# Kernel tuning notes

Hardware: AMD Instinct MI355X
Metric: run time of the kernel (lower is better)

Reference implementation:

```python
import math
import jax, jax.numpy as jnp
import numpy as np

NUM_ANGLE = 8
NUM_RADIAL = 3
RADIAL_MIN = 0.08
RADIAL_MAX = 0.9
EPS = 1e-6


def _hann(n):
    # torch.hann_window(n, periodic=False)
    return 0.5 * (1.0 - jnp.cos(2.0 * jnp.pi * jnp.arange(n, dtype=jnp.float32) / (n - 1)))


def _to_luma(img):
    # img: [B, 3, H, W] -> [B, H, W]
    return 0.2989 * img[:, 0] + 0.587 * img[:, 1] + 0.114 * img[:, 2]


def _log_magnitude(img):
    x = _to_luma(img).astype(jnp.float32)  # [B, H, W]
    H, W = x.shape[-2], x.shape[-1]
    win = _hann(H)[:, None] * _hann(W)[None, :]  # [H, W]
    x = x * win
    spec = jnp.fft.fftshift(jnp.fft.fft2(x, axes=(-2, -1)), axes=(-2, -1))
    return jnp.log1p(jnp.abs(spec))  # [B, H, W]


def _polar_masks(H, W):
    y = jnp.linspace(-1.0, 1.0, H, dtype=jnp.float32)
    x = jnp.linspace(-1.0, 1.0, W, dtype=jnp.float32)
    yy, xx = jnp.meshgrid(y, x, indexing='ij')
    radius = jnp.sqrt(xx * xx + yy * yy)
    radius = radius / jnp.maximum(radius.max(), EPS)
    angle = jnp.remainder(jnp.arctan2(yy, xx), math.pi)

    r_edges = jnp.linspace(RADIAL_MIN, RADIAL_MAX, NUM_RADIAL + 1, dtype=jnp.float32)
    a_edges = jnp.linspace(0.0, math.pi, NUM_ANGLE + 1, dtype=jnp.float32)

    r0 = r_edges[:-1][:, None, None]
    r1 = r_edges[1:][:, None, None]
    rmask = (radius[None] >= r0) & (radius[None] < r1)           # [R, H, W]
    rmask = rmask.at[-1].set((radius >= r_edges[-2]) & (radius <= r_edges[-1]))

    t0 = a_edges[:-1][:, None, None]
    t1 = a_edges[1:][:, None, None]
    amask = (angle[None] >= t0) & (angle[None] < t1)             # [A, H, W]
    amask = amask.at[-1].set((angle >= a_edges[-2]) & (angle <= a_edges[-1]))

    return (rmask[:, None] & amask[None, :]).astype(jnp.float32)  # [R, A, H, W]


def _sector_energies(img):
    mag = _log_magnitude(img)                          # [B, H, W]
    masks = _polar_masks(mag.shape[-2], mag.shape[-1])  # [R, A, H, W]
    mask_sum = jnp.maximum(masks.sum(axis=(-2, -1)), EPS)        # [R, A]
    masked_sum = jnp.einsum('bhw,rahw->bra', mag, masks)         # [B, R, A]
    energies = masked_sum / mask_sum[None]
    energies = energies / jnp.maximum(energies.sum(axis=-1, keepdims=True), EPS)
    return energies


def setup_inputs() -> dict:
    key = jax.random.key(0)
    k1, k2 = jax.random.split(key)
    B, C, H, W = 16, 3, 512, 512
    prediction = jax.random.uniform(k1, (B, C, H, W), dtype=jnp.float32)
    target = jax.random.uniform(k2, (B, C, H, W), dtype=jnp.float32)
    radial_weights = jnp.array([0.5, 1.0, 1.2], dtype=jnp.float32).reshape(1, NUM_RADIAL, 1)
    return {"prediction": prediction, "target": target, "radial_weights": radial_weights}


def reference(prediction, target, radial_weights):
    pred_e = _sector_energies(prediction)   # [B, R, A]
    tgt_e = _sector_energies(target)
    diff = pred_e - tgt_e
    dist = jnp.sqrt(diff * diff + EPS)      # charbonnier
    return (dist * radial_weights).mean()
```

## Files before the change

### kernel.cpp

```cpp
#include <hip/hip_runtime.h>
#include <math.h>

#define PI_F 3.14159265358979323846f
#define TWO_PI_F 6.28318530717958647692f
#define RSQ2 0.70710678118654752440f

#define LGKM(n) __asm__ volatile("s_waitcnt lgkmcnt(" #n ")" ::: "memory")
#define LADDR(a) ((a) + ((a) >> 3))

__device__ __forceinline__ float2 cadd(float2 a, float2 b){ return make_float2(a.x+b.x, a.y+b.y); }
__device__ __forceinline__ float2 csub(float2 a, float2 b){ return make_float2(a.x-b.x, a.y-b.y); }
__device__ __forceinline__ float2 cmul(float2 a, float2 b){ return make_float2(a.x*b.x - a.y*b.y, a.x*b.y + a.y*b.x); }
__device__ __forceinline__ float2 cw1(float2 a){ return make_float2(RSQ2*(a.x+a.y), RSQ2*(a.y-a.x)); }
__device__ __forceinline__ float2 cw2(float2 a){ return make_float2(a.y, -a.x); }
__device__ __forceinline__ float2 cw3(float2 a){ return make_float2(RSQ2*(a.y-a.x), -RSQ2*(a.x+a.y)); }

__device__ __forceinline__ void dft8(float2* v){
    float2 a0=cadd(v[0],v[4]), a1=cadd(v[1],v[5]), a2=cadd(v[2],v[6]), a3=cadd(v[3],v[7]);
    float2 b0=csub(v[0],v[4]);
    float2 b1=cw1(csub(v[1],v[5]));
    float2 b2=cw2(csub(v[2],v[6]));
    float2 b3=cw3(csub(v[3],v[7]));
    float2 c0=cadd(a0,a2), c2=csub(a0,a2), c1=cadd(a1,a3), c3=cw2(csub(a1,a3));
    float2 d0=cadd(b0,b2), d2=csub(b0,b2), d1=cadd(b1,b3), d3=cw2(csub(b1,b3));
    v[0]=cadd(c0,c1); v[1]=csub(c0,c1);
    v[2]=cadd(c2,c3); v[3]=csub(c2,c3);
    v[4]=cadd(d0,d1); v[5]=csub(d0,d1);
    v[6]=cadd(d2,d3); v[7]=csub(d2,d3);
}

__device__ __forceinline__ void calc_pows(float2 w, float2* p){
    p[0] = w;
    p[1] = cmul(w, w);
    p[2] = cmul(p[1], w);
    p[3] = cmul(p[1], p[1]);
    p[4] = cmul(p[2], p[1]);
    p[5] = cmul(p[2], p[2]);
    p[6] = cmul(p[3], p[2]);
}

__device__ __forceinline__ void stage_store(float2* wl, const float2* v, const float2* p,
                                            int base, int step){
    constexpr int br[8] = {0,4,2,6,1,5,3,7};
    wl[LADDR(base)] = v[0];
    #pragma unroll
    for (int c = 1; c < 8; ++c) wl[LADDR(base + step*c)] = cmul(v[br[c]], p[c-1]);
}

__device__ __forceinline__ void stage_load(const float2* wl, float2* v, int j){
    #pragma unroll
    for (int i = 0; i < 8; ++i) v[i] = wl[LADDR(j + 64*i)];
}

__device__ __forceinline__ void fft512_pair(float2* va, float2* vb,
                                            float2* wlA, float2* wlB,
                                            float2 tw0, float2 tw1, int j){
    float2 pw[7];
    calc_pows(tw0, pw);
    dft8(va);
    dft8(vb);
    stage_store(wlA, va, pw, 8 * j, 1);
    stage_store(wlB, vb, pw, 8 * j, 1);
    LGKM(8);
    stage_load(wlA, va, j);
    LGKM(8);
    stage_load(wlB, vb, j);
    LGKM(8);
    calc_pows(tw1, pw);
    dft8(va);
    stage_store(wlA, va, pw, (j & 7) + 64 * (j >> 3), 8);
    LGKM(8);
    dft8(vb);
    stage_store(wlB, vb, pw, (j & 7) + 64 * (j >> 3), 8);
    LGKM(8);
    stage_load(wlA, va, j);
    LGKM(8);
    stage_load(wlB, vb, j);
    LGKM(8);
    dft8(va);
    LGKM(0);
    dft8(vb);
}

__device__ __forceinline__ int sector_id(int hm, int wm) {
    const float step = 2.0f / 511.0f;
    float y = -1.0f + step * (float)hm;
    float x = -1.0f + step * (float)wm;
    float radius = sqrtf(x * x + y * y);
    float r = radius / sqrtf(2.0f);
    float a = atan2f(y, x);
    a = fmodf(a, PI_F);
    if (a < 0.0f) a += PI_F;

    const float rstep = (0.9f - 0.08f) / 3.0f;
    const float re0 = 0.08f;
    const float re1 = 0.08f + rstep;
    const float re2 = 0.08f + 2.0f * rstep;
    const float re3 = 0.9f;
    int rb;
    if      (r >= re0 && r < re1)  rb = 0;
    else if (r >= re1 && r < re2)  rb = 1;
    else if (r >= re2 && r <= re3) rb = 2;
    else return -1;

    const float astep = PI_F / 8.0f;
    int ab = 7;
    #pragma unroll
    for (int i = 0; i < 7; ++i) {
        float t0 = astep * (float)i;
        float t1 = astep * (float)(i + 1);
        if (a >= t0 && a < t1) { ab = i; break; }
    }
    return rb * 8 + ab;
}

__device__ __forceinline__ float hannf(int i) {
    return 0.5f * (1.0f - __cosf(TWO_PI_F * (float)i / 511.0f));
}

__device__ __forceinline__ float lumaf(const float* b, size_t off){
    return 0.2989f*b[off] + 0.587f*b[off+262144] + 0.114f*b[off+524288];
}

__device__ __forceinline__ void write_row_T(float4* __restrict__ out4, size_t ibase, int hp,
                                            const float2* v, int partner, int j){
    constexpr int br[8] = {0,4,2,6,1,5,3,7};
    float4* row = out4 + (ibase + (size_t)hp) * 256;
    #pragma unroll
    for (int c = 0; c < 4; ++c) {
        int k = j + 64 * c;
        float2 zk = v[br[c]];
        float mx = __shfl(v[br[7 - c]].x, partner, 64);
        float my = __shfl(v[br[7 - c]].y, partner, 64);
        float2 zs = v[br[(8 - c) & 7]];
        float2 zm = make_float2(j == 0 ? zs.x : mx, j == 0 ? zs.y : my);
        float4 o = make_float4(0.5f*(zk.x+zm.x), 0.5f*(zk.y-zm.y),
                               0.5f*(zk.y+zm.y), 0.5f*(zm.x-zk.x));
        if (k != 0) row[k] = o;
    }
    if (j == 0) {
        float2 z0 = v[br[0]], z4 = v[br[4]];
        row[0] = make_float4(z0.x, z4.x, z0.y, z4.y);
    }
}

__device__ __forceinline__ void bin_col(const float2* v,
                                        const unsigned char* __restrict__ mw1,
                                        const unsigned char* __restrict__ mw2,
                                        float* wb, int rep, int j){
    constexpr int br[8] = {0,4,2,6,1,5,3,7};
    #pragma unroll
    for (int c = 0; c < 8; ++c) {
        float2 z = v[br[c]];
        float mag = __logf(1.0f + sqrtf(z.x * z.x + z.y * z.y));
        int hm = j + 64 * ((c + 4) & 7);
        int s1 = mw1[hm]; if (s1 < 24) atomicAdd(&wb[rep + s1], mag);
        int hm2 = (256 - (j + 64 * c)) & 511;
        int s2 = mw2[hm2]; if (s2 < 24) atomicAdd(&wb[rep + s2], mag);
    }
}

__global__ __launch_bounds__(256, 4) void rowfft_kernel(const float* __restrict__ pred,
                                                        const float* __restrict__ tgt,
                                                        float4* __restrict__ out4,
                                                        unsigned char* __restrict__ mapT,
                                                        unsigned short* __restrict__ cnt_u16,
                                                        float* __restrict__ acc_rep) {
    __shared__ float2 lds[4 * 1152];
    __shared__ float cbins[24];
    int blk = blockIdx.x;
    int img = blk >> 5;
    int pb  = blk & 31;
    int t = threadIdx.x;
    int wv = t >> 6, j = t & 63;
    int hpA = pb * 8 + wv * 2;
    int hpB = hpA + 1;
    int h0 = 2 * hpA;
    float2* wlA = lds + wv * 1152;
    float2* wlB = wlA + 576;

    if (blk < 48) acc_rep[blk * 256 + t] = 0.0f;
    if (t < 24) cbins[t] = 0.0f;
    __syncthreads();
    {
        int idx = blk * 256 + t;
        int wm = idx >> 9, hm = idx & 511;
        int s = sector_id(hm, wm);
        mapT[idx] = (unsigned char)(s < 0 ? 255 : s);
        if (s >= 0) atomicAdd(&cbins[s], 1.0f);
    }

    const float* base = (img < 16) ? (pred + (size_t)img * 786432)
                                   : (tgt  + (size_t)(img - 16) * 786432);
    float whA0 = hannf(h0), whA1 = hannf(h0 + 1);
    float whB0 = hannf(h0 + 2), whB1 = hannf(h0 + 3);
    float2 va[8], vb[8];
    #pragma unroll
    for (int i = 0; i < 8; ++i) {
        int w = j + 64 * i;
        float ww = hannf(w);
        size_t off0 = (size_t)h0 * 512 + w;
        float l0 = lumaf(base, off0);
        float l1 = lumaf(base, off0 + 512);
        float l2 = lumaf(base, off0 + 1024);
        float l3 = lumaf(base, off0 + 1536);
        va[i] = make_float2(l0 * (whA0 * ww), l1 * (whA1 * ww));
        vb[i] = make_float2(l2 * (whB0 * ww), l3 * (whB1 * ww));
    }

    float sn, cs;
    __sincosf(-TWO_PI_F * (float)j / 512.0f, &sn, &cs);
    float2 tw0 = make_float2(cs, sn);
    __sincosf(-TWO_PI_F * (float)((j >> 3) << 3) / 512.0f, &sn, &cs);
    float2 tw1 = make_float2(cs, sn);

    fft512_pair(va, vb, wlA, wlB, tw0, tw1, j);

    size_t ibase = (size_t)img * 256;
    int partner = (64 - j) & 63;
    write_row_T(out4, ibase, hpA, va, partner, j);
    write_row_T(out4, ibase, hpB, vb, partner, j);

    __syncthreads();
    if (t < 24) cnt_u16[t * 1024 + blk] = (unsigned short)(int)cbins[t];
}

__global__ __launch_bounds__(256, 4) void colfft_kernel(const float4* __restrict__ buf4,
                                                        const unsigned char* __restrict__ mapT,
                                                        float* __restrict__ acc_rep) {
    __shared__ float2 lds[4 * 1152];
    int blk = blockIdx.x;
    int t = threadIdx.x;
    int wv = t >> 6, j = t & 63;
    int img = blk >> 5;
    int b8  = blk & 31;
    int wA = b8 * 8 + wv * 2, wB = wA + 1;
    int pg = blk * 4 + wv;
    float2* wlA = lds + wv * 1152;
    float2* wlB = wlA + 576;

    const float4* b4 = buf4 + ((size_t)img * 256) * 256 + wA;
    float2 va[8], vb[8];
    #pragma unroll
    for (int i = 0; i < 8; ++i) {
        int h = j + 64 * i;
        const float4* row = b4 + (size_t)(h >> 1) * 256;
        float4 q0 = row[0], q1 = row[1];
        bool odd = (h & 1) != 0;
        va[i] = odd ? make_float2(q0.z, q0.w) : make_float2(q0.x, q0.y);
        vb[i] = odd ? make_float2(q1.z, q1.w) : make_float2(q1.x, q1.y);
    }

    float sn, cs;
    __sincosf(-TWO_PI_F * (float)j / 512.0f, &sn, &cs);
    float2 tw0 = make_float2(cs, sn);
    __sincosf(-TWO_PI_F * (float)((j >> 3) << 3) / 512.0f, &sn, &cs);
    float2 tw1 = make_float2(cs, sn);

    fft512_pair(va, vb, wlA, wlB, tw0, tw1, j);

    float* wb = (float*)wlA;
    #pragma unroll
    for (int i = 0; i < 4; ++i) { int ii = j + 64 * i; if (ii < 200) wb[ii] = 0.0f; }
    LGKM(0);

    constexpr int br[8] = {0,4,2,6,1,5,3,7};
    int rep = (j & 7) * 25;
    bool pairw = (wA == 0);
    if (pairw) {
        int partner = (64 - j) & 63;
        const unsigned char* mwA1 = mapT + (size_t)256 * 512;
        const unsigned char* mwA2 = mapT;
        #pragma unroll
        for (int c = 0; c < 8; ++c) {
            float2 zk = va[br[c]];
            float mx = __shfl(va[br[7 - c]].x, partner, 64);
            float my = __shfl(va[br[7 - c]].y, partner, 64);
            float2 zs = va[br[(8 - c) & 7]];
            float2 zm = make_float2(j == 0 ? zs.x : mx, j == 0 ? zs.y : my);
            float f0x = 0.5f*(zk.x+zm.x), f0y = 0.5f*(zk.y-zm.y);
            float f1x = 0.5f*(zk.y+zm.y), f1y = 0.5f*(zm.x-zk.x);
            float mag0 = __logf(1.0f + sqrtf(f0x*f0x + f0y*f0y));
            float mag1 = __logf(1.0f + sqrtf(f1x*f1x + f1y*f1y));
            int hm = j + 64 * ((c + 4) & 7);
            int s1 = mwA1[hm]; if (s1 < 24) atomicAdd(&wb[rep + s1], mag0);
            int s2 = mwA2[hm]; if (s2 < 24) atomicAdd(&wb[rep + s2], mag1);
        }
    } else {
        bin_col(va, mapT + (size_t)((wA + 256) & 511) * 512,
                    mapT + (size_t)((256 - wA) & 511) * 512, wb, rep, j);
    }
    bin_col(vb, mapT + (size_t)((wB + 256) & 511) * 512,
                mapT + (size_t)((256 - wB) & 511) * 512, wb, rep, j);
    LGKM(0);
    if (j < 24) {
        float sum = 0.0f;
        #pragma unroll
        for (int r = 0; r < 8; ++r) sum += wb[r * 25 + j];
        atomicAdd(&acc_rep[(pg & 15) * 768 + img * 24 + j], sum);
    }
}

__global__ __launch_bounds__(256) void final_kernel(const float* __restrict__ acc_rep,
                                                    const unsigned short* __restrict__ cnt_u16,
                                                    const float* __restrict__ rw,
                                                    float* __restrict__ out) {
    __shared__ float accs[768];
    __shared__ float cnts[24];
    __shared__ float ep[384], et[384], red[384];
    int t = threadIdx.x;
    for (int o = t; o < 768; o += 256) {
        float s = 0.0f;
        #pragma unroll
        for (int r = 0; r < 16; ++r) s += acc_rep[r * 768 + o];
        accs[o] = s;
    }
    if (t < 192) {
        int s = t >> 3, g = t & 7;
        const ushort4* p = (const ushort4*)(cnt_u16 + s * 1024 + g * 128);
        float sum = 0.0f;
        #pragma unroll
        for (int i = 0; i < 32; ++i) { ushort4 u = p[i]; sum += (float)(u.x + u.y + u.z + u.w); }
        sum += __shfl_down(sum, 4, 8);
        sum += __shfl_down(sum, 2, 8);
        sum += __shfl_down(sum, 1, 8);
        if (g == 0) cnts[s] = sum;
    }
    __syncthreads();
    for (int idx = t; idx < 384; idx += 256) {
        int b = idx / 24, s = idx - b * 24;
        float cnt = fmaxf(cnts[s], 1e-6f);
        ep[idx] = accs[b * 24 + s] / cnt;
        et[idx] = accs[(16 + b) * 24 + s] / cnt;
    }
    __syncthreads();
    for (int idx = t; idx < 384; idx += 256) {
        int b = idx / 24, s = idx - b * 24, r = s >> 3;
        int gbase = b * 24 + r * 8;
        float sp = 0.0f, st = 0.0f;
        #pragma unroll
        for (int a = 0; a < 8; ++a) { sp += ep[gbase + a]; st += et[gbase + a]; }
        float pe = ep[idx] / fmaxf(sp, 1e-6f);
        float te = et[idx] / fmaxf(st, 1e-6f);
        float d = pe - te;
        red[idx] = sqrtf(d * d + 1e-6f) * rw[r];
    }
    __syncthreads();
    if (t < 128) red[t] += red[t + 128] + red[t + 256];
    __syncthreads();
    if (t < 64) {
        float vv = red[t] + red[t + 64];
        #pragma unroll
        for (int o = 32; o > 0; o >>= 1) vv += __shfl_down(vv, o, 64);
        if (t == 0) out[0] = vv / 384.0f;
    }
}

extern "C" void kernel_launch(void* const* d_in, const int* in_sizes, int n_in,
                              void* d_out, int out_size, void* d_ws, size_t ws_size,
                              hipStream_t stream) {
    const float* pred = (const float*)d_in[0];
    const float* tgt  = (const float*)d_in[1];
    const float* rw   = (const float*)d_in[2];

    char* ws = (char*)d_ws;
    float* acc_rep       = (float*)ws;
    unsigned short* cnt  = (unsigned short*)(ws + 49152);
    unsigned char* mapT  = (unsigned char*)(ws + 98304);
    float4* buf4         = (float4*)(ws + 360448);

    rowfft_kernel<<<1024, 256, 0, stream>>>(pred, tgt, buf4, mapT, cnt, acc_rep);
    colfft_kernel<<<1024, 256, 0, stream>>>(buf4, mapT, acc_rep);
    final_kernel<<<1, 256, 0, stream>>>(acc_rep, cnt, rw, (float*)d_out);
}
```

Before: 187.0 us.

## Stage column-FFT input through LDS and prefetch sector map bytes early

The column FFT kernel now loads its 8-column strip of the transposed spectrum cooperatively into padded shared memory with coalesced reads, then each wave picks out its columns from LDS instead of doing strided 32-byte global reads per element. The sector-index bytes from the mask map are loaded into registers before the FFT, so their latency overlaps compute rather than stalling the binning loop. The row kernel's launch bound occupancy hint drops from 4 to 3. This costs an extra block barrier and more registers for the prefetched indices.

```diff
diff --git a/kernel.cpp b/kernel.cpp
--- a/kernel.cpp
+++ b/kernel.cpp
@@ -144,29 +144,13 @@
     }
 }
 
-__device__ __forceinline__ void bin_col(const float2* v,
-                                        const unsigned char* __restrict__ mw1,
-                                        const unsigned char* __restrict__ mw2,
-                                        float* wb, int rep, int j){
-    constexpr int br[8] = {0,4,2,6,1,5,3,7};
-    #pragma unroll
-    for (int c = 0; c < 8; ++c) {
-        float2 z = v[br[c]];
-        float mag = __logf(1.0f + sqrtf(z.x * z.x + z.y * z.y));
-        int hm = j + 64 * ((c + 4) & 7);
-        int s1 = mw1[hm]; if (s1 < 24) atomicAdd(&wb[rep + s1], mag);
-        int hm2 = (256 - (j + 64 * c)) & 511;
-        int s2 = mw2[hm2]; if (s2 < 24) atomicAdd(&wb[rep + s2], mag);
-    }
-}
-
-__global__ __launch_bounds__(256, 4) void rowfft_kernel(const float* __restrict__ pred,
+__global__ __launch_bounds__(256, 3) void rowfft_kernel(const float* __restrict__ pred,
                                                         const float* __restrict__ tgt,
                                                         float4* __restrict__ out4,
                                                         unsigned char* __restrict__ mapT,
                                                         unsigned short* __restrict__ cnt_u16,
                                                         float* __restrict__ acc_rep) {
-    __shared__ float2 lds[4 * 1152];
+    __shared__ __align__(16) float2 lds[4 * 1152];
     __shared__ float cbins[24];
     int blk = blockIdx.x;
     int img = blk >> 5;
@@ -228,28 +212,62 @@
 __global__ __launch_bounds__(256, 4) void colfft_kernel(const float4* __restrict__ buf4,
                                                         const unsigned char* __restrict__ mapT,
                                                         float* __restrict__ acc_rep) {
-    __shared__ float2 lds[4 * 1152];
+    __shared__ __align__(16) float2 lds[4 * 1152];
     int blk = blockIdx.x;
     int t = threadIdx.x;
     int wv = t >> 6, j = t & 63;
     int img = blk >> 5;
     int b8  = blk & 31;
-    int wA = b8 * 8 + wv * 2, wB = wA + 1;
+    int w0  = b8 * 8;
+    int wA = w0 + wv * 2, wB = wA + 1;
     int pg = blk * 4 + wv;
     float2* wlA = lds + wv * 1152;
     float2* wlB = wlA + 576;
 
-    const float4* b4 = buf4 + ((size_t)img * 256) * 256 + wA;
+    {
+        const float4* src = buf4 + ((size_t)img * 256) * 256 + w0;
+        float4* stg = (float4*)lds;
+        int rr = t >> 3, cc = t & 7;
+        #pragma unroll
+        for (int it = 0; it < 8; ++it) {
+            int hp = it * 32 + rr;
+            stg[hp * 9 + cc] = src[(size_t)hp * 256 + cc];
+        }
+    }
+    __syncthreads();
+
     float2 va[8], vb[8];
-    #pragma unroll
-    for (int i = 0; i < 8; ++i) {
-        int h = j + 64 * i;
-        const float4* row = b4 + (size_t)(h >> 1) * 256;
-        float4 q0 = row[0], q1 = row[1];
-        bool odd = (h & 1) != 0;
-        va[i] = odd ? make_float2(q0.z, q0.w) : make_float2(q0.x, q0.y);
-        vb[i] = odd ? make_float2(q1.z, q1.w) : make_float2(q1.x, q1.y);
-    }
+    {
+        const float4* stg = (const float4*)lds;
+        #pragma unroll
+        for (int i = 0; i < 8; ++i) {
+            int h = j + 64 * i;
+            int hp = h >> 1;
+            bool odd = (h & 1) != 0;
+            float4 qa = stg[hp * 9 + wv * 2];
+            float4 qb = stg[hp * 9 + wv * 2 + 1];
+            va[i] = odd ? make_float2(qa.z, qa.w) : make_float2(qa.x, qa.y);
+            vb[i] = odd ? make_float2(qb.z, qb.w) : make_float2(qb.x, qb.y);
+        }
+    }
+
+    bool pairw = (wA == 0);
+    const unsigned char* mwA1 = mapT + (size_t)(pairw ? 256 : ((wA + 256) & 511)) * 512;
+    const unsigned char* mwA2 = mapT + (size_t)(pairw ? 0   : ((256 - wA) & 511)) * 512;
+    const unsigned char* mwB1 = mapT + (size_t)((wB + 256) & 511) * 512;
+    const unsigned char* mwB2 = mapT + (size_t)((256 - wB) & 511) * 512;
+    unsigned char sA1[8], sA2[8], sB1[8], sB2[8];
+    #pragma unroll
+    for (int c = 0; c < 8; ++c) {
+        int hm = j + 64 * ((c + 4) & 7);
+        int hm2 = (256 - (j + 64 * c)) & 511;
+        sA1[c] = mwA1[hm];
+        sA2[c] = pairw ? mwA2[hm] : mwA2[hm2];
+        sB1[c] = mwB1[hm];
+        sB2[c] = mwB2[hm2];
+    }
+
+    __syncthreads();
 
     float sn, cs;
     __sincosf(-TWO_PI_F * (float)j / 512.0f, &sn, &cs);
@@ -266,11 +284,8 @@
 
     constexpr int br[8] = {0,4,2,6,1,5,3,7};
     int rep = (j & 7) * 25;
-    bool pairw = (wA == 0);
     if (pairw) {
         int partner = (64 - j) & 63;
-        const unsigned char* mwA1 = mapT + (size_t)256 * 512;
-        const unsigned char* mwA2 = mapT;
         #pragma unroll
         for (int c = 0; c < 8; ++c) {
             float2 zk = va[br[c]];
@@ -282,16 +297,25 @@
             float f1x = 0.5f*(zk.y+zm.y), f1y = 0.5f*(zm.x-zk.x);
             float mag0 = __logf(1.0f + sqrtf(f0x*f0x + f0y*f0y));
             float mag1 = __logf(1.0f + sqrtf(f1x*f1x + f1y*f1y));
-            int hm = j + 64 * ((c + 4) & 7);
-            int s1 = mwA1[hm]; if (s1 < 24) atomicAdd(&wb[rep + s1], mag0);
-            int s2 = mwA2[hm]; if (s2 < 24) atomicAdd(&wb[rep + s2], mag1);
+            int s1 = sA1[c]; if (s1 < 24) atomicAdd(&wb[rep + s1], mag0);
+            int s2 = sA2[c]; if (s2 < 24) atomicAdd(&wb[rep + s2], mag1);
         }
     } else {
-        bin_col(va, mapT + (size_t)((wA + 256) & 511) * 512,
-                    mapT + (size_t)((256 - wA) & 511) * 512, wb, rep, j);
-    }
-    bin_col(vb, mapT + (size_t)((wB + 256) & 511) * 512,
-                mapT + (size_t)((256 - wB) & 511) * 512, wb, rep, j);
+        #pragma unroll
+        for (int c = 0; c < 8; ++c) {
+            float2 z = va[br[c]];
+            float mag = __logf(1.0f + sqrtf(z.x * z.x + z.y * z.y));
+            int s1 = sA1[c]; if (s1 < 24) atomicAdd(&wb[rep + s1], mag);
+            int s2 = sA2[c]; if (s2 < 24) atomicAdd(&wb[rep + s2], mag);
+        }
+    }
+    #pragma unroll
+    for (int c = 0; c < 8; ++c) {
+        float2 z = vb[br[c]];
+        float mag = __logf(1.0f + sqrtf(z.x * z.x + z.y * z.y));
+        int s1 = sB1[c]; if (s1 < 24) atomicAdd(&wb[rep + s1], mag);
+        int s2 = sB2[c]; if (s2 < 24) atomicAdd(&wb[rep + s2], mag);
+    }
     LGKM(0);
     if (j < 24) {
         float sum = 0.0f;
```

Result: slower. 193.8 us (+3.7%).

## Split column FFT binning into magnitude write plus separate coalesced bin kernel

Applied to the files above, without the earlier changes.

The column FFT kernel no longer bins magnitudes with scattered byte-map lookups and LDS atomics. It now writes the full log-magnitude image to a workspace buffer, and a new bin kernel reads the magnitudes and the mask map contiguously with vector loads before accumulating sector sums. This replaces gathered mask reads and divergent atomic binning inside the FFT kernel. In exchange it adds a 32 MB global write and read round trip, the write pattern is scattered across mirrored rows, and there is an extra kernel launch.

```diff
diff --git a/kernel.cpp b/kernel.cpp
--- a/kernel.cpp
+++ b/kernel.cpp
@@ -144,29 +144,13 @@
     }
 }
 
-__device__ __forceinline__ void bin_col(const float2* v,
-                                        const unsigned char* __restrict__ mw1,
-                                        const unsigned char* __restrict__ mw2,
-                                        float* wb, int rep, int j){
-    constexpr int br[8] = {0,4,2,6,1,5,3,7};
-    #pragma unroll
-    for (int c = 0; c < 8; ++c) {
-        float2 z = v[br[c]];
-        float mag = __logf(1.0f + sqrtf(z.x * z.x + z.y * z.y));
-        int hm = j + 64 * ((c + 4) & 7);
-        int s1 = mw1[hm]; if (s1 < 24) atomicAdd(&wb[rep + s1], mag);
-        int hm2 = (256 - (j + 64 * c)) & 511;
-        int s2 = mw2[hm2]; if (s2 < 24) atomicAdd(&wb[rep + s2], mag);
-    }
-}
-
 __global__ __launch_bounds__(256, 4) void rowfft_kernel(const float* __restrict__ pred,
                                                         const float* __restrict__ tgt,
                                                         float4* __restrict__ out4,
                                                         unsigned char* __restrict__ mapT,
                                                         unsigned short* __restrict__ cnt_u16,
                                                         float* __restrict__ acc_rep) {
-    __shared__ float2 lds[4 * 1152];
+    __shared__ __align__(16) float2 lds[4 * 1152];
     __shared__ float cbins[24];
     int blk = blockIdx.x;
     int img = blk >> 5;
@@ -225,17 +209,15 @@
     if (t < 24) cnt_u16[t * 1024 + blk] = (unsigned short)(int)cbins[t];
 }
 
-__global__ __launch_bounds__(256, 4) void colfft_kernel(const float4* __restrict__ buf4,
-                                                        const unsigned char* __restrict__ mapT,
-                                                        float* __restrict__ acc_rep) {
-    __shared__ float2 lds[4 * 1152];
+__global__ __launch_bounds__(256, 4) void magfft_kernel(const float4* __restrict__ buf4,
+                                                        float* __restrict__ magbuf) {
+    __shared__ __align__(16) float2 lds[4 * 1152];
     int blk = blockIdx.x;
     int t = threadIdx.x;
     int wv = t >> 6, j = t & 63;
     int img = blk >> 5;
     int b8  = blk & 31;
     int wA = b8 * 8 + wv * 2, wB = wA + 1;
-    int pg = blk * 4 + wv;
     float2* wlA = lds + wv * 1152;
     float2* wlB = wlA + 576;
 
@@ -259,18 +241,11 @@
 
     fft512_pair(va, vb, wlA, wlB, tw0, tw1, j);
 
-    float* wb = (float*)wlA;
-    #pragma unroll
-    for (int i = 0; i < 4; ++i) { int ii = j + 64 * i; if (ii < 200) wb[ii] = 0.0f; }
-    LGKM(0);
-
     constexpr int br[8] = {0,4,2,6,1,5,3,7};
-    int rep = (j & 7) * 25;
+    float* mgi = magbuf + ((size_t)img << 18);
     bool pairw = (wA == 0);
     if (pairw) {
         int partner = (64 - j) & 63;
-        const unsigned char* mwA1 = mapT + (size_t)256 * 512;
-        const unsigned char* mwA2 = mapT;
         #pragma unroll
         for (int c = 0; c < 8; ++c) {
             float2 zk = va[br[c]];
@@ -283,21 +258,67 @@
             float mag0 = __logf(1.0f + sqrtf(f0x*f0x + f0y*f0y));
             float mag1 = __logf(1.0f + sqrtf(f1x*f1x + f1y*f1y));
             int hm = j + 64 * ((c + 4) & 7);
-            int s1 = mwA1[hm]; if (s1 < 24) atomicAdd(&wb[rep + s1], mag0);
-            int s2 = mwA2[hm]; if (s2 < 24) atomicAdd(&wb[rep + s2], mag1);
+            mgi[(256 << 9) + hm] = mag0;
+            mgi[hm] = mag1;
         }
     } else {
-        bin_col(va, mapT + (size_t)((wA + 256) & 511) * 512,
-                    mapT + (size_t)((256 - wA) & 511) * 512, wb, rep, j);
-    }
-    bin_col(vb, mapT + (size_t)((wB + 256) & 511) * 512,
-                mapT + (size_t)((256 - wB) & 511) * 512, wb, rep, j);
-    LGKM(0);
-    if (j < 24) {
+        int wm1 = wA + 256;
+        int wm2 = 256 - wA;
+        #pragma unroll
+        for (int c = 0; c < 8; ++c) {
+            float2 z = va[br[c]];
+            float mag = __logf(1.0f + sqrtf(z.x * z.x + z.y * z.y));
+            int hm = j + 64 * ((c + 4) & 7);
+            int hm2 = (256 - (j + 64 * c)) & 511;
+            mgi[(wm1 << 9) + hm] = mag;
+            mgi[(wm2 << 9) + hm2] = mag;
+        }
+    }
+    {
+        int wm1 = wB + 256;
+        int wm2 = 256 - wB;
+        #pragma unroll
+        for (int c = 0; c < 8; ++c) {
+            float2 z = vb[br[c]];
+            float mag = __logf(1.0f + sqrtf(z.x * z.x + z.y * z.y));
+            int hm = j + 64 * ((c + 4) & 7);
+            int hm2 = (256 - (j + 64 * c)) & 511;
+            mgi[(wm1 << 9) + hm] = mag;
+            mgi[(wm2 << 9) + hm2] = mag;
+        }
+    }
+}
+
+__global__ __launch_bounds__(256, 8) void bin_kernel(const float* __restrict__ magbuf,
+                                                     const unsigned char* __restrict__ mapT,
+                                                     float* __restrict__ acc_rep) {
+    __shared__ float wb[200];
+    int blk = blockIdx.x;
+    int t = threadIdx.x;
+    int img = blk >> 6;
+    int seg = blk & 63;
+    for (int i = t; i < 200; i += 256) wb[i] = 0.0f;
+    __syncthreads();
+    int rep = (t & 7) * 25;
+    const float4* m4 = (const float4*)(magbuf + ((size_t)img << 18) + ((size_t)seg << 12));
+    const uint4*  p4 = (const uint4*)(mapT + ((size_t)seg << 12));
+    uint4 mp = p4[t];
+    float4 v0 = m4[t * 4 + 0], v1 = m4[t * 4 + 1];
+    float4 v2 = m4[t * 4 + 2], v3 = m4[t * 4 + 3];
+    unsigned mw[4] = {mp.x, mp.y, mp.z, mp.w};
+    float vv[16] = {v0.x, v0.y, v0.z, v0.w, v1.x, v1.y, v1.z, v1.w,
+                    v2.x, v2.y, v2.z, v2.w, v3.x, v3.y, v3.z, v3.w};
+    #pragma unroll
+    for (int q = 0; q < 16; ++q) {
+        int s = (mw[q >> 2] >> ((q & 3) * 8)) & 255;
+        if (s < 24) atomicAdd(&wb[rep + s], vv[q]);
+    }
+    __syncthreads();
+    if (t < 24) {
         float sum = 0.0f;
         #pragma unroll
-        for (int r = 0; r < 8; ++r) sum += wb[r * 25 + j];
-        atomicAdd(&acc_rep[(pg & 15) * 768 + img * 24 + j], sum);
+        for (int r = 0; r < 8; ++r) sum += wb[r * 25 + t];
+        atomicAdd(&acc_rep[(blk & 15) * 768 + img * 24 + t], sum);
     }
 }
 
@@ -368,8 +389,10 @@
     unsigned short* cnt  = (unsigned short*)(ws + 49152);
     unsigned char* mapT  = (unsigned char*)(ws + 98304);
     float4* buf4         = (float4*)(ws + 360448);
+    float* magbuf        = (float*)(ws + 33914880);
 
     rowfft_kernel<<<1024, 256, 0, stream>>>(pred, tgt, buf4, mapT, cnt, acc_rep);
-    colfft_kernel<<<1024, 256, 0, stream>>>(buf4, mapT, acc_rep);
+    magfft_kernel<<<1024, 256, 0, stream>>>(buf4, magbuf);
+    bin_kernel<<<2048, 256, 0, stream>>>(magbuf, mapT, acc_rep);
     final_kernel<<<1, 256, 0, stream>>>(acc_rep, cnt, rw, (float*)d_out);
 }
```

Result: no change. 187.4 us (+0.2%).
